# Kernel optimization log

Measured on AMD Instinct MI355X. Metric: run time of the kernel, lower is better.

## Reference

```python
import jax, jax.numpy as jnp
import numpy as np

NH, NOPE_D, ROPE_D, V_D, R = 16, 48, 16, 64, 128
EPS = 1e-6

def rms_norm(x, w):
    norm = jax.lax.rsqrt(jnp.mean(jnp.square(x), axis=-1, keepdims=True) + EPS)
    return x * norm * w

def apply_rope(x, cos, sin):
    # x: (..., rope_d); cos/sin broadcastable (..., rope_d//2)
    d = x.shape[-1]
    x1, x2 = x[..., : d // 2], x[..., d // 2 :]
    return jnp.concatenate([x1 * cos - x2 * sin, x2 * cos + x1 * sin], axis=-1)

def setup_inputs() -> dict:
    key = jax.random.key(0)
    ks = jax.random.split(key, 8)
    B, T, D = 2, 2048, 1024
    s = lambda fan_in: 1.0 / np.sqrt(fan_in)
    return {
        "x": jax.random.normal(ks[0], (B, T, D), jnp.float32),
        "cos": jax.random.uniform(ks[1], (T, ROPE_D // 2), jnp.float32),
        "sin": jax.random.uniform(ks[2], (T, ROPE_D // 2), jnp.float32),
        "Wq": jax.random.normal(ks[3], (NH * (NOPE_D + ROPE_D), D), jnp.float32) * s(D),
        "q_norm_w": jnp.ones((NOPE_D + ROPE_D,), jnp.float32),
        "Wkva": jax.random.normal(ks[4], (R + ROPE_D, D), jnp.float32) * s(D),
        "kva_norm_w": jnp.ones((R,), jnp.float32),
        "Wkvb": jax.random.normal(ks[5], (NH * (NOPE_D + V_D), R), jnp.float32) * s(R),
        "Wo": jax.random.normal(ks[6], (D, NH * V_D), jnp.float32) * s(NH * V_D),
    }

def reference(x, cos, sin, Wq, q_norm_w, Wkva, kva_norm_w, Wkvb, Wo):
    B, T, D = x.shape
    # Q path: project, per-head RMSNorm over (nope+rope) dims, split
    q = (x @ Wq.T).reshape(B, T, NH, NOPE_D + ROPE_D)
    q = rms_norm(q, q_norm_w)
    q_nope, q_rope = q[..., :NOPE_D], q[..., NOPE_D:]
    # Low-rank KV path
    kv_a = x @ Wkva.T  # (B,T,R+ROPE_D)
    kv_latent = rms_norm(kv_a[..., :R], kva_norm_w)
    k_rope_raw = kv_a[..., R:]  # (B,T,ROPE_D) shared across heads
    kv_b = (kv_latent @ Wkvb.T).reshape(B, T, NH, NOPE_D + V_D)
    k_nope, v = kv_b[..., :NOPE_D], kv_b[..., NOPE_D:]
    # Decoupled RoPE
    cos_t = cos[None, :T, None, :]  # (1,T,1,rope_d/2)
    sin_t = sin[None, :T, None, :]
    q_rope = apply_rope(q_rope, cos_t, sin_t)
    k_rope = apply_rope(k_rope_raw[:, :, None, :], cos[None, :T, None, :], sin[None, :T, None, :])
    k_rope = jnp.broadcast_to(k_rope, (B, T, NH, ROPE_D))
    q_full = jnp.concatenate([q_nope, q_rope], axis=-1)  # (B,T,NH,64)
    k_full = jnp.concatenate([k_nope, k_rope], axis=-1)
    # Causal attention, scale = 1/sqrt(nope+rope)
    scale = (NOPE_D + ROPE_D) ** -0.5
    scores = jnp.einsum("bqhd,bkhd->bhqk", q_full, k_full) * scale
    causal = jnp.tril(jnp.ones((T, T), bool))
    scores = jnp.where(causal[None, None], scores, -jnp.inf)
    attn = jax.nn.softmax(scores, axis=-1)
    out = jnp.einsum("bhqk,bkhd->bqhd", attn, v).reshape(B, T, NH * V_D)
    return out @ Wo.T
```

## Files before the change

### kernel.cpp

```cpp
#include <hip/hip_runtime.h>
#include <hip/hip_bf16.h>
#include <math.h>

#define NH 16
#define T_ 2048
#define B_ 2
#define D_ 1024
#define EPS 1e-6f

typedef __attribute__((ext_vector_type(8))) short bf16x8;
typedef __attribute__((ext_vector_type(4))) float f32x4;

__device__ __forceinline__ float wred_sum(float v){
  #pragma unroll
  for (int o = 32; o > 0; o >>= 1) v += __shfl_xor(v, o, 64);
  return v;
}

__device__ __forceinline__ unsigned pack_bf16(float a, float b){
  __hip_bfloat162 t = __float22bfloat162_rn(make_float2(a, b));
  unsigned r; __builtin_memcpy(&r, &t, 4); return r;
}

__device__ __forceinline__ void gload_lds16(const void* g, void* l){
  __builtin_amdgcn_global_load_lds((const __attribute__((address_space(1))) void*)g,
                                   (__attribute__((address_space(3))) void*)l, 16, 0, 0);
}

__global__ __launch_bounds__(256)
void cvt5(const float* __restrict__ x, const float* __restrict__ wq,
          const float* __restrict__ wkva, const float* __restrict__ wkvb,
          const float* __restrict__ wo,
          __hip_bfloat16* __restrict__ xb, __hip_bfloat16* __restrict__ wqb,
          __hip_bfloat16* __restrict__ wkvab, __hip_bfloat16* __restrict__ wkvbb,
          __hip_bfloat16* __restrict__ wob)
{
  const int i = blockIdx.x * 256 + threadIdx.x;
  const float* s; __hip_bfloat16* d; int off;
  if      (i < 1048576) { s = x;    d = xb;    off = i; }
  else if (i < 1310720) { s = wq;   d = wqb;   off = i - 1048576; }
  else if (i < 1347584) { s = wkva; d = wkvab; off = i - 1310720; }
  else if (i < 1404928) { s = wkvb; d = wkvbb; off = i - 1347584; }
  else                  { s = wo;   d = wob;   off = i - 1404928; }
  float4 v = *(const float4*)(s + (size_t)off * 4);
  *(__hip_bfloat162*)(d + (size_t)off * 4)     = __float22bfloat162_rn(make_float2(v.x, v.y));
  *(__hip_bfloat162*)(d + (size_t)off * 4 + 2) = __float22bfloat162_rn(make_float2(v.z, v.w));
}

template<typename CT>
__global__ __launch_bounds__(256, 2)
void gemm_bt64(const __hip_bfloat16* __restrict__ A, const __hip_bfloat16* __restrict__ W,
               CT* __restrict__ C, int M, int N, int K)
{
  __shared__ __hip_bfloat16 As[128 * 64];
  __shared__ __hip_bfloat16 Ws[64 * 64];
  const int tid = threadIdx.x;
  const int wv = tid >> 6, lane = tid & 63;
  const int m = lane & 15, quad = lane >> 4;
  const int bm = blockIdx.y * 128, bn = blockIdx.x * 64;

  const __hip_bfloat16* ga[4];
  const __hip_bfloat16* gw[2];
  #pragma unroll
  for (int i = 0; i < 4; i++) {
    const int slot = i*256 + tid;
    const int row = slot >> 3, cb = slot & 7;
    ga[i] = A + (size_t)(bm + row) * K + ((cb ^ (row & 7)) << 3);
  }
  #pragma unroll
  for (int i = 0; i < 2; i++) {
    const int slot = i*256 + tid;
    const int row = slot >> 3, cb = slot & 7;
    int wr = bn + row; if (wr >= N) wr = N - 1;
    gw[i] = W + (size_t)wr * K + ((cb ^ (row & 7)) << 3);
  }

  f32x4 acc[2][4];
  #pragma unroll
  for (int mi = 0; mi < 2; mi++)
    #pragma unroll
    for (int nj = 0; nj < 4; nj++) acc[mi][nj] = (f32x4){0.f,0.f,0.f,0.f};

  for (int k0 = 0; k0 < K; k0 += 64) {
    #pragma unroll
    for (int i = 0; i < 4; i++) {
      gload_lds16(ga[i], As + (i*256 + wv*64)*8);
      ga[i] += 64;
    }
    #pragma unroll
    for (int i = 0; i < 2; i++) {
      gload_lds16(gw[i], Ws + (i*256 + wv*64)*8);
      gw[i] += 64;
    }
    __syncthreads();
    #pragma unroll
    for (int ks = 0; ks < 2; ks++) {
      const int cb = ((ks*4 + quad) ^ (m & 7)) << 3;
      bf16x8 af[2], wf[4];
      #pragma unroll
      for (int mi = 0; mi < 2; mi++)
        af[mi] = *(const bf16x8*)(As + (wv*32 + mi*16 + m) * 64 + cb);
      #pragma unroll
      for (int nj = 0; nj < 4; nj++)
        wf[nj] = *(const bf16x8*)(Ws + (nj*16 + m) * 64 + cb);
      #pragma unroll
      for (int mi = 0; mi < 2; mi++)
        #pragma unroll
        for (int nj = 0; nj < 4; nj++)
          acc[mi][nj] = __builtin_amdgcn_mfma_f32_16x16x32_bf16(af[mi], wf[nj], acc[mi][nj], 0, 0, 0);
    }
    __syncthreads();
  }

  #pragma unroll
  for (int mi = 0; mi < 2; mi++)
    #pragma unroll
    for (int nj = 0; nj < 4; nj++) {
      const int col = bn + nj*16 + m;
      if (col < N) {
        #pragma unroll
        for (int r = 0; r < 4; r++) {
          const int row = bm + wv*32 + mi*16 + quad*4 + r;
          if constexpr (sizeof(CT) == 2)
            C[(size_t)row * N + col] = (CT)__float2bfloat16(acc[mi][nj][r]);
          else
            C[(size_t)row * N + col] = acc[mi][nj][r];
        }
      }
    }
}

__global__ __launch_bounds__(256, 2)
void gemm_q_fused(const __hip_bfloat16* __restrict__ A, const __hip_bfloat16* __restrict__ W,
                  const float* __restrict__ qw, const float* __restrict__ cosp,
                  const float* __restrict__ sinp, __hip_bfloat16* __restrict__ qb)
{
  __shared__ __hip_bfloat16 As[128 * 64];
  __shared__ __hip_bfloat16 Ws[64 * 64];
  const int K = 1024;
  const int tid = threadIdx.x;
  const int wv = tid >> 6, lane = tid & 63;
  const int m = lane & 15, quad = lane >> 4;
  const int bm = blockIdx.y * 128;
  const int head = blockIdx.x;
  const int bn = head * 64;

  const __hip_bfloat16* ga[4];
  const __hip_bfloat16* gw[2];
  #pragma unroll
  for (int i = 0; i < 4; i++) {
    const int slot = i*256 + tid;
    const int row = slot >> 3, cb = slot & 7;
    ga[i] = A + (size_t)(bm + row) * K + ((cb ^ (row & 7)) << 3);
  }
  #pragma unroll
  for (int i = 0; i < 2; i++) {
    const int slot = i*256 + tid;
    const int row = slot >> 3, cb = slot & 7;
    gw[i] = W + (size_t)(bn + row) * K + ((cb ^ (row & 7)) << 3);
  }

  f32x4 acc[2][4];
  #pragma unroll
  for (int mi = 0; mi < 2; mi++)
    #pragma unroll
    for (int nj = 0; nj < 4; nj++) acc[mi][nj] = (f32x4){0.f,0.f,0.f,0.f};

  for (int k0 = 0; k0 < K; k0 += 64) {
    #pragma unroll
    for (int i = 0; i < 4; i++) { gload_lds16(ga[i], As + (i*256 + wv*64)*8); ga[i] += 64; }
    #pragma unroll
    for (int i = 0; i < 2; i++) { gload_lds16(gw[i], Ws + (i*256 + wv*64)*8); gw[i] += 64; }
    __syncthreads();
    #pragma unroll
    for (int ks = 0; ks < 2; ks++) {
      const int cb = ((ks*4 + quad) ^ (m & 7)) << 3;
      bf16x8 af[2], wf[4];
      #pragma unroll
      for (int mi = 0; mi < 2; mi++)
        af[mi] = *(const bf16x8*)(As + (wv*32 + mi*16 + m) * 64 + cb);
      #pragma unroll
      for (int nj = 0; nj < 4; nj++)
        wf[nj] = *(const bf16x8*)(Ws + (nj*16 + m) * 64 + cb);
      #pragma unroll
      for (int mi = 0; mi < 2; mi++)
        #pragma unroll
        for (int nj = 0; nj < 4; nj++)
          acc[mi][nj] = __builtin_amdgcn_mfma_f32_16x16x32_bf16(af[mi], wf[nj], acc[mi][nj], 0, 0, 0);
    }
    __syncthreads();
  }

  float qwv[4];
  #pragma unroll
  for (int nj = 0; nj < 4; nj++) qwv[nj] = qw[nj*16 + m];
  const int j = m & 7;
  #pragma unroll
  for (int mi = 0; mi < 2; mi++) {
    #pragma unroll
    for (int r = 0; r < 4; r++) {
      float ss = 0.f;
      #pragma unroll
      for (int nj = 0; nj < 4; nj++) { const float t = acc[mi][nj][r]; ss = fmaf(t, t, ss); }
      ss += __shfl_xor(ss, 1, 64); ss += __shfl_xor(ss, 2, 64);
      ss += __shfl_xor(ss, 4, 64); ss += __shfl_xor(ss, 8, 64);
      const float nrm = rsqrtf(ss * (1.0f/64.0f) + EPS);
      float v[4];
      #pragma unroll
      for (int nj = 0; nj < 4; nj++) v[nj] = acc[mi][nj][r] * nrm * qwv[nj];
      const int grow = bm + wv*32 + mi*16 + quad*4 + r;
      const int t = grow & (T_ - 1);
      const int b = grow >> 11;
      const float part = __shfl_xor(v[3], 8, 64);
      const float c = cosp[t*8 + j], sn = sinp[t*8 + j];
      v[3] = (m < 8) ? (v[3]*c - part*sn) : (v[3]*c + part*sn);
      __hip_bfloat16* dst = qb + ((size_t)(b*NH + head)*T_ + t)*64 + m;
      #pragma unroll
      for (int nj = 0; nj < 4; nj++) dst[nj*16] = __float2bfloat16(v[nj] * 0.125f);
    }
  }
}

__global__ void prep_kv(const float* __restrict__ kva, const float* __restrict__ kw,
                        const float* __restrict__ cosp, const float* __restrict__ sinp,
                        __hip_bfloat16* __restrict__ kvl16, __hip_bfloat16* __restrict__ krope16)
{
  const int tid = threadIdx.x;
  const int bt = blockIdx.x;
  const int t = bt % T_;
  const float* row = kva + (size_t)bt * 144;
  const float v = row[tid];
  float s = wred_sum(v * v);
  __shared__ float red[2];
  if ((tid & 63) == 0) red[tid >> 6] = s;
  __syncthreads();
  const float total = red[0] + red[1];
  const float norm = rsqrtf(total * (1.0f/128.0f) + EPS);
  kvl16[(size_t)bt * 128 + tid] = __float2bfloat16(v * norm * kw[tid]);
  if (tid < 16) {
    const int j = tid & 7;
    const float c = cosp[t*8 + j], sn = sinp[t*8 + j];
    const float x1 = row[128 + j], x2 = row[136 + j];
    krope16[(size_t)bt * 16 + tid] = __float2bfloat16((tid < 8) ? (x1 * c - x2 * sn)
                                                               : (x2 * c + x1 * sn));
  }
}

__global__ __launch_bounds__(256)
void pack_v(const __hip_bfloat16* __restrict__ kvb16, __hip_bfloat16* __restrict__ vt)
{
  __shared__ short Vl[64][72];
  const int tid = threadIdx.x;
  const int t0 = blockIdx.x * 64;
  const int bh = blockIdx.y;
  const int b = bh >> 4, h = bh & 15;
  const int r = tid >> 2, c = tid & 3;
  {
    const short* src = (const short*)(kvb16 + ((size_t)(b*T_ + t0 + r)*1792 + h*112 + 48 + c*16));
    union { bf16x8 v; short e[8]; } u0, u1;
    u0.v = *(const bf16x8*)src;
    u1.v = *(const bf16x8*)(src + 8);
    #pragma unroll
    for (int jj = 0; jj < 8; jj++) { Vl[r][c*16+jj] = u0.e[jj]; Vl[r][c*16+8+jj] = u1.e[jj]; }
  }
  __syncthreads();
  const int d = tid >> 2, tq = tid & 3;
  union { bf16x8 v; short e[8]; } o0, o1;
  #pragma unroll
  for (int jj = 0; jj < 8; jj++) { o0.e[jj] = Vl[tq*16+jj][d]; o1.e[jj] = Vl[tq*16+8+jj][d]; }
  short* dst = (short*)(vt + ((size_t)bh*64 + d)*T_ + t0 + tq*16);
  *(bf16x8*)dst = o0.v;
  *(bf16x8*)(dst + 8) = o1.v;
}

__device__ __forceinline__ void fa_softmax(f32x4 (&s)[8], const bool diag,
    const int k0, const int qglob, const int m, const int quad,
    float& mrun, float& lrun, f32x4 (&o)[4], bf16x8 (&a)[4])
{
  if (diag) {
    #pragma unroll
    for (int sub = 0; sub < 8; sub++)
      #pragma unroll
      for (int r = 0; r < 4; r++)
        if (k0 + sub*16 + quad*4 + r > qglob) s[sub][r] = -1e30f;
  }
  float tm = -3.0e38f;
  #pragma unroll
  for (int sub = 0; sub < 8; sub++)
    #pragma unroll
    for (int r = 0; r < 4; r++) tm = fmaxf(tm, s[sub][r]);
  tm = fmaxf(tm, __shfl_xor(tm, 16, 64));
  tm = fmaxf(tm, __shfl_xor(tm, 32, 64));
  const float mn = fmaxf(mrun, tm);
  const float alpha = __expf(mrun - mn);
  float rs = 0.f;
  float p[8][4];
  #pragma unroll
  for (int sub = 0; sub < 8; sub++)
    #pragma unroll
    for (int r = 0; r < 4; r++) {
      const float e = __expf(s[sub][r] - mn);
      p[sub][r] = e; rs += e;
    }
  rs += __shfl_xor(rs, 16, 64);
  rs += __shfl_xor(rs, 32, 64);
  lrun = lrun * alpha + rs;
  mrun = mn;

  unsigned u[8][2];
  #pragma unroll
  for (int sub = 0; sub < 8; sub++) {
    u[sub][0] = pack_bf16(p[sub][0], p[sub][1]);
    u[sub][1] = pack_bf16(p[sub][2], p[sub][3]);
  }
  #pragma unroll
  for (int c = 0; c < 4; c++) {
    union { int i[4]; bf16x8 v; } au;
    #pragma unroll
    for (int w4 = 0; w4 < 4; w4++) {
      const int src = (((2*quad + (w4 >> 1)) & 3) << 4) | m;
      const int lo = __shfl((int)u[c*2][w4 & 1], src, 64);
      const int hi = __shfl((int)u[c*2+1][w4 & 1], src, 64);
      au.i[w4] = (quad & 2) ? hi : lo;
    }
    a[c] = au.v;
  }

  float al[4];
  #pragma unroll
  for (int r = 0; r < 4; r++) al[r] = __shfl(alpha, (quad << 2) | r, 64);
  #pragma unroll
  for (int vs = 0; vs < 4; vs++)
    #pragma unroll
    for (int r = 0; r < 4; r++) o[vs][r] *= al[r];
}

__device__ __forceinline__ void fa_store(float lrun, f32x4 (&oacc)[4],
    const int b, const int qrow0, const int h, const int m, const int quad,
    __hip_bfloat16* __restrict__ aout)
{
  float lr[4];
  #pragma unroll
  for (int r = 0; r < 4; r++) lr[r] = __shfl(lrun, (quad << 2) | r, 64);
  #pragma unroll
  for (int vs = 0; vs < 4; vs++)
    #pragma unroll
    for (int r = 0; r < 4; r++)
      aout[(size_t)(b*T_ + qrow0 + quad*4 + r) * 1024 + h*64 + vs*16 + m]
          = __float2bfloat16(oacc[vs][r] / lr[r]);
}

__global__ __launch_bounds__(256, 2)
void attn_pair2(const __hip_bfloat16* __restrict__ qb,
                const __hip_bfloat16* __restrict__ kvb16,
                const __hip_bfloat16* __restrict__ krope16,
                const __hip_bfloat16* __restrict__ vt16,
                __hip_bfloat16* __restrict__ aout)
{
  __shared__ __hip_bfloat16 SL[32768];
  const int tid = threadIdx.x;
  const int wv = tid >> 6, lane = tid & 63;
  const int m = lane & 15, quad = lane >> 4;
  const int ta = blockIdx.x;
  const int tb = 31 - ta;
  const int bh = blockIdx.y;
  const int b = bh >> 4, h = bh & 15;
  const int qbaseA = ta*64 + wv*16;
  const int qbaseB = tb*64 + wv*16;
  const int ntA = (ta + 2) >> 1;
  const int ntB = (tb + 2) >> 1;

  const __hip_bfloat16* qra = qb + ((size_t)bh*T_ + qbaseA + m)*64 + quad*8;
  const bf16x8 qA0 = *(const bf16x8*)qra, qA1 = *(const bf16x8*)(qra + 32);
  const __hip_bfloat16* qrb = qb + ((size_t)bh*T_ + qbaseB + m)*64 + quad*8;
  const bf16x8 qB0 = *(const bf16x8*)qrb, qB1 = *(const bf16x8*)(qrb + 32);

  const __hip_bfloat16* pK[4]; size_t iK[4];
  const __hip_bfloat16* pV[4];
  #pragma unroll
  for (int i = 0; i < 4; i++) {
    const int slot = i*256 + tid;
    const int krow = slot >> 3;
    const int kde = (slot & 7) ^ (krow & 7);
    if (kde < 6) { pK[i] = kvb16 + (size_t)(b*T_ + krow)*1792 + h*112 + kde*8; iK[i] = (size_t)128*1792; }
    else         { pK[i] = krope16 + (size_t)(b*T_ + krow)*16 + (kde-6)*8;     iK[i] = (size_t)128*16; }
    const int vd = slot >> 4;
    const int vde = (slot & 15) ^ (vd & 7);
    pV[i] = vt16 + ((size_t)bh*64 + vd)*T_ + vde*8;
  }

  auto stage = [&](int buf){
    #pragma unroll
    for (int i = 0; i < 4; i++) {
      gload_lds16(pK[i], SL + buf*8192 + (i*256 + wv*64)*8);
      gload_lds16(pV[i], SL + 16384 + buf*8192 + (i*256 + wv*64)*8);
      pK[i] += iK[i]; pV[i] += 128;
    }
  };

  f32x4 oA[4], oB[4];
  #pragma unroll
  for (int vs = 0; vs < 4; vs++) { oA[vs] = (f32x4){0.f,0.f,0.f,0.f}; oB[vs] = (f32x4){0.f,0.f,0.f,0.f}; }
  float mA = -3.0e38f, lA = 0.f, mB = -3.0e38f, lB = 0.f;

  const int sw0 = quad ^ (m & 7);
  stage(0);

  for (int kt = 0; kt < ntB; kt++) {
    const int cur = kt & 1;
    __syncthreads();
    const __hip_bfloat16* Kc = SL + cur*8192;
    const __hip_bfloat16* Vc = SL + 16384 + cur*8192;
    const bool doA = (kt < ntA);

    f32x4 sA[8], sB[8];
    #pragma unroll
    for (int sub = 0; sub < 8; sub++) {
      const bf16x8 kf0 = *(const bf16x8*)(Kc + (sub*16 + m)*64 + sw0*8);
      const bf16x8 kf1 = *(const bf16x8*)(Kc + (sub*16 + m)*64 + (sw0^4)*8);
      f32x4 z = (f32x4){0.f,0.f,0.f,0.f};
      z = __builtin_amdgcn_mfma_f32_16x16x32_bf16(kf0, qB0, z, 0, 0, 0);
      z = __builtin_amdgcn_mfma_f32_16x16x32_bf16(kf1, qB1, z, 0, 0, 0);
      sB[sub] = z;
      if (doA) {
        f32x4 y = (f32x4){0.f,0.f,0.f,0.f};
        y = __builtin_amdgcn_mfma_f32_16x16x32_bf16(kf0, qA0, y, 0, 0, 0);
        y = __builtin_amdgcn_mfma_f32_16x16x32_bf16(kf1, qA1, y, 0, 0, 0);
        sA[sub] = y;
      }
    }

    if (kt + 1 < ntB) stage(cur ^ 1);

    bf16x8 aA[4], aB[4];
    fa_softmax(sB, kt == ntB-1, kt*128, qbaseB + m, m, quad, mB, lB, oB, aB);
    if (doA) fa_softmax(sA, kt == ntA-1, kt*128, qbaseA + m, m, quad, mA, lA, oA, aA);

    #pragma unroll
    for (int vs = 0; vs < 4; vs++) {
      #pragma unroll
      for (int c = 0; c < 4; c++) {
        const bf16x8 vf = *(const bf16x8*)(Vc + (vs*16 + m)*128 + (((c*4 + quad) ^ (m & 7)) << 3));
        oB[vs] = __builtin_amdgcn_mfma_f32_16x16x32_bf16(aB[c], vf, oB[vs], 0, 0, 0);
        if (doA) oA[vs] = __builtin_amdgcn_mfma_f32_16x16x32_bf16(aA[c], vf, oA[vs], 0, 0, 0);
      }
    }
  }

  fa_store(lA, oA, b, qbaseA, h, m, quad, aout);
  fa_store(lB, oB, b, qbaseB, h, m, quad, aout);
}

extern "C" void kernel_launch(void* const* d_in, const int* in_sizes, int n_in,
                              void* d_out, int out_size, void* d_ws, size_t ws_size,
                              hipStream_t stream)
{
  const float* x    = (const float*)d_in[0];
  const float* cosp = (const float*)d_in[1];
  const float* sinp = (const float*)d_in[2];
  const float* Wq   = (const float*)d_in[3];
  const float* qw   = (const float*)d_in[4];
  const float* Wkva = (const float*)d_in[5];
  const float* kw   = (const float*)d_in[6];
  const float* Wkvb = (const float*)d_in[7];
  const float* Wo   = (const float*)d_in[8];
  float* out = (float*)d_out;

  float* kva = (float*)d_ws;
  __hip_bfloat16* kvb16   = (__hip_bfloat16*)(kva + 589824);
  __hip_bfloat16* kvl16   = kvb16 + 7340032;
  __hip_bfloat16* qb16    = kvl16 + 524288;
  __hip_bfloat16* vt16    = qb16 + 4194304;
  __hip_bfloat16* krope16 = vt16 + 4194304;
  __hip_bfloat16* Wqb     = krope16 + 65536;
  __hip_bfloat16* Wkvab   = Wqb + 1048576;
  __hip_bfloat16* Wkvbb   = Wkvab + 147456;
  __hip_bfloat16* Wob     = Wkvbb + 229376;
  __hip_bfloat16* ab16    = Wob + 1048576;
  __hip_bfloat16* xb16    = kvb16;

  const int M = B_ * T_;

  cvt5<<<6512, 256, 0, stream>>>(x, Wq, Wkva, Wkvb, Wo, xb16, Wqb, Wkvab, Wkvbb, Wob);
  gemm_q_fused<<<dim3(16, 32), 256, 0, stream>>>(xb16, Wqb, qw, cosp, sinp, qb16);
  gemm_bt64<float><<<dim3(3, 32), 256, 0, stream>>>(xb16, Wkvab, kva, M, 144, 1024);
  prep_kv<<<M, 128, 0, stream>>>(kva, kw, cosp, sinp, kvl16, krope16);
  gemm_bt64<__hip_bfloat16><<<dim3(28, 32), 256, 0, stream>>>(kvl16, Wkvbb, kvb16, M, 1792, 128);
  pack_v<<<dim3(T_/64, B_ * NH), 256, 0, stream>>>(kvb16, vt16);
  attn_pair2<<<dim3(16, B_ * NH), 256, 0, stream>>>(qb16, kvb16, krope16, vt16, ab16);
  gemm_bt64<float><<<dim3(16, 32), 256, 0, stream>>>(ab16, Wob, out, M, 1024, 1024);
}
```

Baseline: 209.7 us.

## Fuse Q and KV-A GEMMs, double-buffer GEMMs, fuse V transpose into KV-B GEMM

Merges the Q projection and the KV-A projection into one launch that picks its weight matrix by block index. All GEMMs now double-buffer their LDS tiles, so the next K slice loads while the current one computes, and one barrier per iteration is removed. Wkvb rows are permuted during the bf16 conversion so the KV-B GEMM writes k_nope as a compact array and writes V already transposed through LDS. This removes the separate pack_v kernel and the large kvb intermediate. The cost is twice the LDS per block, which may lower occupancy, plus a more involved epilogue.

```diff
diff --git a/kernel.cpp b/kernel.cpp
--- a/kernel.cpp
+++ b/kernel.cpp
@@ -36,15 +36,21 @@
           __hip_bfloat16* __restrict__ wob)
 {
   const int i = blockIdx.x * 256 + threadIdx.x;
-  const float* s; __hip_bfloat16* d; int off;
-  if      (i < 1048576) { s = x;    d = xb;    off = i; }
-  else if (i < 1310720) { s = wq;   d = wqb;   off = i - 1048576; }
-  else if (i < 1347584) { s = wkva; d = wkvab; off = i - 1310720; }
-  else if (i < 1404928) { s = wkvb; d = wkvbb; off = i - 1347584; }
-  else                  { s = wo;   d = wob;   off = i - 1404928; }
-  float4 v = *(const float4*)(s + (size_t)off * 4);
-  *(__hip_bfloat162*)(d + (size_t)off * 4)     = __float22bfloat162_rn(make_float2(v.x, v.y));
-  *(__hip_bfloat162*)(d + (size_t)off * 4 + 2) = __float22bfloat162_rn(make_float2(v.z, v.w));
+  const float* s; __hip_bfloat16* d; size_t soff, doff;
+  if      (i < 1048576) { s = x;    d = xb;    soff = doff = i; }
+  else if (i < 1310720) { s = wq;   d = wqb;   soff = doff = i - 1048576; }
+  else if (i < 1347584) { s = wkva; d = wkvab; soff = doff = i - 1310720; }
+  else if (i < 1404928) {
+    const int off = i - 1347584;
+    const int srow = off >> 5, c4 = off & 31;
+    const int h = srow / 112, dd = srow % 112;
+    const int drow = (dd < 48) ? (h*48 + dd) : (768 + h*64 + (dd - 48));
+    s = wkvb; d = wkvbb; soff = off; doff = (size_t)drow*32 + c4;
+  }
+  else                  { s = wo;   d = wob;   soff = doff = i - 1404928; }
+  float4 v = *(const float4*)(s + soff * 4);
+  *(__hip_bfloat162*)(d + doff * 4)     = __float22bfloat162_rn(make_float2(v.x, v.y));
+  *(__hip_bfloat162*)(d + doff * 4 + 2) = __float22bfloat162_rn(make_float2(v.z, v.w));
 }
 
 template<typename CT>
@@ -52,8 +58,8 @@
 void gemm_bt64(const __hip_bfloat16* __restrict__ A, const __hip_bfloat16* __restrict__ W,
                CT* __restrict__ C, int M, int N, int K)
 {
-  __shared__ __hip_bfloat16 As[128 * 64];
-  __shared__ __hip_bfloat16 Ws[64 * 64];
+  __shared__ __hip_bfloat16 As[2][128 * 64];
+  __shared__ __hip_bfloat16 Ws[2][64 * 64];
   const int tid = threadIdx.x;
   const int wv = tid >> 6, lane = tid & 63;
   const int m = lane & 15, quad = lane >> 4;
@@ -74,6 +80,12 @@
     int wr = bn + row; if (wr >= N) wr = N - 1;
     gw[i] = W + (size_t)wr * K + ((cb ^ (row & 7)) << 3);
   }
+  auto stage = [&](int buf){
+    #pragma unroll
+    for (int i = 0; i < 4; i++) { gload_lds16(ga[i], &As[buf][(i*256 + wv*64)*8]); ga[i] += 64; }
+    #pragma unroll
+    for (int i = 0; i < 2; i++) { gload_lds16(gw[i], &Ws[buf][(i*256 + wv*64)*8]); gw[i] += 64; }
+  };
 
   f32x4 acc[2][4];
   #pragma unroll
@@ -81,35 +93,28 @@
     #pragma unroll
     for (int nj = 0; nj < 4; nj++) acc[mi][nj] = (f32x4){0.f,0.f,0.f,0.f};
 
-  for (int k0 = 0; k0 < K; k0 += 64) {
-    #pragma unroll
-    for (int i = 0; i < 4; i++) {
-      gload_lds16(ga[i], As + (i*256 + wv*64)*8);
-      ga[i] += 64;
-    }
-    #pragma unroll
-    for (int i = 0; i < 2; i++) {
-      gload_lds16(gw[i], Ws + (i*256 + wv*64)*8);
-      gw[i] += 64;
-    }
+  stage(0);
+  const int iters = K >> 6;
+  for (int it = 0; it < iters; it++) {
+    const int cur = it & 1;
     __syncthreads();
+    if (it + 1 < iters) stage(cur ^ 1);
     #pragma unroll
     for (int ks = 0; ks < 2; ks++) {
       const int cb = ((ks*4 + quad) ^ (m & 7)) << 3;
       bf16x8 af[2], wf[4];
       #pragma unroll
       for (int mi = 0; mi < 2; mi++)
-        af[mi] = *(const bf16x8*)(As + (wv*32 + mi*16 + m) * 64 + cb);
+        af[mi] = *(const bf16x8*)(&As[cur][(wv*32 + mi*16 + m) * 64 + cb]);
       #pragma unroll
       for (int nj = 0; nj < 4; nj++)
-        wf[nj] = *(const bf16x8*)(Ws + (nj*16 + m) * 64 + cb);
+        wf[nj] = *(const bf16x8*)(&Ws[cur][(nj*16 + m) * 64 + cb]);
       #pragma unroll
       for (int mi = 0; mi < 2; mi++)
         #pragma unroll
         for (int nj = 0; nj < 4; nj++)
           acc[mi][nj] = __builtin_amdgcn_mfma_f32_16x16x32_bf16(af[mi], wf[nj], acc[mi][nj], 0, 0, 0);
     }
-    __syncthreads();
   }
 
   #pragma unroll
@@ -131,19 +136,23 @@
 }
 
 __global__ __launch_bounds__(256, 2)
-void gemm_q_fused(const __hip_bfloat16* __restrict__ A, const __hip_bfloat16* __restrict__ W,
-                  const float* __restrict__ qw, const float* __restrict__ cosp,
-                  const float* __restrict__ sinp, __hip_bfloat16* __restrict__ qb)
-{
-  __shared__ __hip_bfloat16 As[128 * 64];
-  __shared__ __hip_bfloat16 Ws[64 * 64];
+void gemm_qkva(const __hip_bfloat16* __restrict__ A, const __hip_bfloat16* __restrict__ Wqb,
+               const __hip_bfloat16* __restrict__ Wkvab,
+               const float* __restrict__ qw, const float* __restrict__ cosp,
+               const float* __restrict__ sinp,
+               __hip_bfloat16* __restrict__ qb, float* __restrict__ kva)
+{
+  __shared__ __hip_bfloat16 As[2][128 * 64];
+  __shared__ __hip_bfloat16 Ws[2][64 * 64];
   const int K = 1024;
   const int tid = threadIdx.x;
   const int wv = tid >> 6, lane = tid & 63;
   const int m = lane & 15, quad = lane >> 4;
   const int bm = blockIdx.y * 128;
-  const int head = blockIdx.x;
-  const int bn = head * 64;
+  const bool isq = blockIdx.x < 16;
+  const __hip_bfloat16* W = isq ? Wqb : Wkvab;
+  const int bn = isq ? blockIdx.x*64 : (blockIdx.x - 16)*64;
+  const int Nw = isq ? 1024 : 144;
 
   const __hip_bfloat16* ga[4];
   const __hip_bfloat16* gw[2];
@@ -157,8 +166,15 @@
   for (int i = 0; i < 2; i++) {
     const int slot = i*256 + tid;
     const int row = slot >> 3, cb = slot & 7;
-    gw[i] = W + (size_t)(bn + row) * K + ((cb ^ (row & 7)) << 3);
-  }
+    int wr = bn + row; if (wr >= Nw) wr = Nw - 1;
+    gw[i] = W + (size_t)wr * K + ((cb ^ (row & 7)) << 3);
+  }
+  auto stage = [&](int buf){
+    #pragma unroll
+    for (int i = 0; i < 4; i++) { gload_lds16(ga[i], &As[buf][(i*256 + wv*64)*8]); ga[i] += 64; }
+    #pragma unroll
+    for (int i = 0; i < 2; i++) { gload_lds16(gw[i], &Ws[buf][(i*256 + wv*64)*8]); gw[i] += 64; }
+  };
 
   f32x4 acc[2][4];
   #pragma unroll
@@ -166,58 +182,73 @@
     #pragma unroll
     for (int nj = 0; nj < 4; nj++) acc[mi][nj] = (f32x4){0.f,0.f,0.f,0.f};
 
-  for (int k0 = 0; k0 < K; k0 += 64) {
-    #pragma unroll
-    for (int i = 0; i < 4; i++) { gload_lds16(ga[i], As + (i*256 + wv*64)*8); ga[i] += 64; }
-    #pragma unroll
-    for (int i = 0; i < 2; i++) { gload_lds16(gw[i], Ws + (i*256 + wv*64)*8); gw[i] += 64; }
+  stage(0);
+  for (int it = 0; it < 16; it++) {
+    const int cur = it & 1;
     __syncthreads();
+    if (it < 15) stage(cur ^ 1);
     #pragma unroll
     for (int ks = 0; ks < 2; ks++) {
       const int cb = ((ks*4 + quad) ^ (m & 7)) << 3;
       bf16x8 af[2], wf[4];
       #pragma unroll
       for (int mi = 0; mi < 2; mi++)
-        af[mi] = *(const bf16x8*)(As + (wv*32 + mi*16 + m) * 64 + cb);
+        af[mi] = *(const bf16x8*)(&As[cur][(wv*32 + mi*16 + m) * 64 + cb]);
       #pragma unroll
       for (int nj = 0; nj < 4; nj++)
-        wf[nj] = *(const bf16x8*)(Ws + (nj*16 + m) * 64 + cb);
+        wf[nj] = *(const bf16x8*)(&Ws[cur][(nj*16 + m) * 64 + cb]);
       #pragma unroll
       for (int mi = 0; mi < 2; mi++)
         #pragma unroll
         for (int nj = 0; nj < 4; nj++)
           acc[mi][nj] = __builtin_amdgcn_mfma_f32_16x16x32_bf16(af[mi], wf[nj], acc[mi][nj], 0, 0, 0);
     }
-    __syncthreads();
-  }
-
-  float qwv[4];
-  #pragma unroll
-  for (int nj = 0; nj < 4; nj++) qwv[nj] = qw[nj*16 + m];
-  const int j = m & 7;
-  #pragma unroll
-  for (int mi = 0; mi < 2; mi++) {
-    #pragma unroll
-    for (int r = 0; r < 4; r++) {
-      float ss = 0.f;
-      #pragma unroll
-      for (int nj = 0; nj < 4; nj++) { const float t = acc[mi][nj][r]; ss = fmaf(t, t, ss); }
-      ss += __shfl_xor(ss, 1, 64); ss += __shfl_xor(ss, 2, 64);
-      ss += __shfl_xor(ss, 4, 64); ss += __shfl_xor(ss, 8, 64);
-      const float nrm = rsqrtf(ss * (1.0f/64.0f) + EPS);
-      float v[4];
-      #pragma unroll
-      for (int nj = 0; nj < 4; nj++) v[nj] = acc[mi][nj][r] * nrm * qwv[nj];
-      const int grow = bm + wv*32 + mi*16 + quad*4 + r;
-      const int t = grow & (T_ - 1);
-      const int b = grow >> 11;
-      const float part = __shfl_xor(v[3], 8, 64);
-      const float c = cosp[t*8 + j], sn = sinp[t*8 + j];
-      v[3] = (m < 8) ? (v[3]*c - part*sn) : (v[3]*c + part*sn);
-      __hip_bfloat16* dst = qb + ((size_t)(b*NH + head)*T_ + t)*64 + m;
-      #pragma unroll
-      for (int nj = 0; nj < 4; nj++) dst[nj*16] = __float2bfloat16(v[nj] * 0.125f);
-    }
+  }
+
+  if (isq) {
+    const int head = blockIdx.x;
+    float qwv[4];
+    #pragma unroll
+    for (int nj = 0; nj < 4; nj++) qwv[nj] = qw[nj*16 + m];
+    const int j = m & 7;
+    #pragma unroll
+    for (int mi = 0; mi < 2; mi++) {
+      #pragma unroll
+      for (int r = 0; r < 4; r++) {
+        float ss = 0.f;
+        #pragma unroll
+        for (int nj = 0; nj < 4; nj++) { const float t = acc[mi][nj][r]; ss = fmaf(t, t, ss); }
+        ss += __shfl_xor(ss, 1, 64); ss += __shfl_xor(ss, 2, 64);
+        ss += __shfl_xor(ss, 4, 64); ss += __shfl_xor(ss, 8, 64);
+        const float nrm = rsqrtf(ss * (1.0f/64.0f) + EPS);
+        float v[4];
+        #pragma unroll
+        for (int nj = 0; nj < 4; nj++) v[nj] = acc[mi][nj][r] * nrm * qwv[nj];
+        const int grow = bm + wv*32 + mi*16 + quad*4 + r;
+        const int t = grow & (T_ - 1);
+        const int b = grow >> 11;
+        const float part = __shfl_xor(v[3], 8, 64);
+        const float c = cosp[t*8 + j], sn = sinp[t*8 + j];
+        v[3] = (m < 8) ? (v[3]*c - part*sn) : (v[3]*c + part*sn);
+        __hip_bfloat16* dst = qb + ((size_t)(b*NH + head)*T_ + t)*64 + m;
+        #pragma unroll
+        for (int nj = 0; nj < 4; nj++) dst[nj*16] = __float2bfloat16(v[nj] * 0.125f);
+      }
+    }
+  } else {
+    #pragma unroll
+    for (int mi = 0; mi < 2; mi++)
+      #pragma unroll
+      for (int nj = 0; nj < 4; nj++) {
+        const int col = bn + nj*16 + m;
+        if (col < 144) {
+          #pragma unroll
+          for (int r = 0; r < 4; r++) {
+            const int row = bm + wv*32 + mi*16 + quad*4 + r;
+            kva[(size_t)row * 144 + col] = acc[mi][nj][r];
+          }
+        }
+      }
   }
 }
 
@@ -246,31 +277,108 @@
   }
 }
 
-__global__ __launch_bounds__(256)
-void pack_v(const __hip_bfloat16* __restrict__ kvb16, __hip_bfloat16* __restrict__ vt)
-{
-  __shared__ short Vl[64][72];
+__global__ __launch_bounds__(256, 2)
+void gemm_kvb(const __hip_bfloat16* __restrict__ A, const __hip_bfloat16* __restrict__ W,
+              __hip_bfloat16* __restrict__ knope, __hip_bfloat16* __restrict__ vt)
+{
+  __shared__ __hip_bfloat16 As[2][128 * 64];
+  __shared__ __hip_bfloat16 Ws[2][64 * 64];
+  const int K = 128;
   const int tid = threadIdx.x;
-  const int t0 = blockIdx.x * 64;
-  const int bh = blockIdx.y;
-  const int b = bh >> 4, h = bh & 15;
-  const int r = tid >> 2, c = tid & 3;
-  {
-    const short* src = (const short*)(kvb16 + ((size_t)(b*T_ + t0 + r)*1792 + h*112 + 48 + c*16));
-    union { bf16x8 v; short e[8]; } u0, u1;
-    u0.v = *(const bf16x8*)src;
-    u1.v = *(const bf16x8*)(src + 8);
-    #pragma unroll
-    for (int jj = 0; jj < 8; jj++) { Vl[r][c*16+jj] = u0.e[jj]; Vl[r][c*16+8+jj] = u1.e[jj]; }
-  }
-  __syncthreads();
-  const int d = tid >> 2, tq = tid & 3;
-  union { bf16x8 v; short e[8]; } o0, o1;
-  #pragma unroll
-  for (int jj = 0; jj < 8; jj++) { o0.e[jj] = Vl[tq*16+jj][d]; o1.e[jj] = Vl[tq*16+8+jj][d]; }
-  short* dst = (short*)(vt + ((size_t)bh*64 + d)*T_ + t0 + tq*16);
-  *(bf16x8*)dst = o0.v;
-  *(bf16x8*)(dst + 8) = o1.v;
+  const int wv = tid >> 6, lane = tid & 63;
+  const int m = lane & 15, quad = lane >> 4;
+  const int bm = blockIdx.y * 128, bn = blockIdx.x * 64;
+
+  const __hip_bfloat16* ga[4];
+  const __hip_bfloat16* gw[2];
+  #pragma unroll
+  for (int i = 0; i < 4; i++) {
+    const int slot = i*256 + tid;
+    const int row = slot >> 3, cb = slot & 7;
+    ga[i] = A + (size_t)(bm + row) * K + ((cb ^ (row & 7)) << 3);
+  }
+  #pragma unroll
+  for (int i = 0; i < 2; i++) {
+    const int slot = i*256 + tid;
+    const int row = slot >> 3, cb = slot & 7;
+    gw[i] = W + (size_t)(bn + row) * K + ((cb ^ (row & 7)) << 3);
+  }
+  auto stage = [&](int buf){
+    #pragma unroll
+    for (int i = 0; i < 4; i++) { gload_lds16(ga[i], &As[buf][(i*256 + wv*64)*8]); ga[i] += 64; }
+    #pragma unroll
+    for (int i = 0; i < 2; i++) { gload_lds16(gw[i], &Ws[buf][(i*256 + wv*64)*8]); gw[i] += 64; }
+  };
+
+  f32x4 acc[2][4];
+  #pragma unroll
+  for (int mi = 0; mi < 2; mi++)
+    #pragma unroll
+    for (int nj = 0; nj < 4; nj++) acc[mi][nj] = (f32x4){0.f,0.f,0.f,0.f};
+
+  stage(0);
+  for (int it = 0; it < 2; it++) {
+    const int cur = it & 1;
+    __syncthreads();
+    if (it == 0) stage(1);
+    #pragma unroll
+    for (int ks = 0; ks < 2; ks++) {
+      const int cb = ((ks*4 + quad) ^ (m & 7)) << 3;
+      bf16x8 af[2], wf[4];
+      #pragma unroll
+      for (int mi = 0; mi < 2; mi++)
+        af[mi] = *(const bf16x8*)(&As[cur][(wv*32 + mi*16 + m) * 64 + cb]);
+      #pragma unroll
+      for (int nj = 0; nj < 4; nj++)
+        wf[nj] = *(const bf16x8*)(&Ws[cur][(nj*16 + m) * 64 + cb]);
+      #pragma unroll
+      for (int mi = 0; mi < 2; mi++)
+        #pragma unroll
+        for (int nj = 0; nj < 4; nj++)
+          acc[mi][nj] = __builtin_amdgcn_mfma_f32_16x16x32_bf16(af[mi], wf[nj], acc[mi][nj], 0, 0, 0);
+    }
+  }
+
+  if (bn < 768) {
+    #pragma unroll
+    for (int mi = 0; mi < 2; mi++)
+      #pragma unroll
+      for (int nj = 0; nj < 4; nj++) {
+        const int col = bn + nj*16 + m;
+        #pragma unroll
+        for (int r = 0; r < 4; r++) {
+          const int row = bm + wv*32 + mi*16 + quad*4 + r;
+          knope[(size_t)row * 768 + col] = __float2bfloat16(acc[mi][nj][r]);
+        }
+      }
+  } else {
+    __syncthreads();
+    short* TL = (short*)&As[0][0];
+    #pragma unroll
+    for (int mi = 0; mi < 2; mi++)
+      #pragma unroll
+      for (int nj = 0; nj < 4; nj++) {
+        const int d = nj*16 + m;
+        #pragma unroll
+        for (int r = 0; r < 4; r++) {
+          const int tl = wv*32 + mi*16 + quad*4 + r;
+          __hip_bfloat16 hv = __float2bfloat16(acc[mi][nj][r]);
+          short sv; __builtin_memcpy(&sv, &hv, 2);
+          TL[d*136 + tl] = sv;
+        }
+      }
+    __syncthreads();
+    const int h = (bn - 768) >> 6;
+    const int b = bm >> 11;
+    const int t0 = bm & (T_ - 1);
+    #pragma unroll
+    for (int i = 0; i < 4; i++) {
+      const int unit = i*256 + tid;
+      const int d = unit >> 4, tu = unit & 15;
+      *(bf16x8*)(vt + ((size_t)(b*NH + h)*64 + d)*T_ + t0 + tu*8)
+          = *(const bf16x8*)(TL + d*136 + tu*8);
+    }
+  }
 }
 
 __device__ __forceinline__ void fa_softmax(f32x4 (&s)[8], const bool diag,
@@ -352,7 +460,7 @@
 
 __global__ __launch_bounds__(256, 2)
 void attn_pair2(const __hip_bfloat16* __restrict__ qb,
-                const __hip_bfloat16* __restrict__ kvb16,
+                const __hip_bfloat16* __restrict__ knope,
                 const __hip_bfloat16* __restrict__ krope16,
                 const __hip_bfloat16* __restrict__ vt16,
                 __hip_bfloat16* __restrict__ aout)
@@ -382,8 +490,8 @@
     const int slot = i*256 + tid;
     const int krow = slot >> 3;
     const int kde = (slot & 7) ^ (krow & 7);
-    if (kde < 6) { pK[i] = kvb16 + (size_t)(b*T_ + krow)*1792 + h*112 + kde*8; iK[i] = (size_t)128*1792; }
-    else         { pK[i] = krope16 + (size_t)(b*T_ + krow)*16 + (kde-6)*8;     iK[i] = (size_t)128*16; }
+    if (kde < 6) { pK[i] = knope + (size_t)(b*T_ + krow)*768 + h*48 + kde*8; iK[i] = (size_t)128*768; }
+    else         { pK[i] = krope16 + (size_t)(b*T_ + krow)*16 + (kde-6)*8;   iK[i] = (size_t)128*16; }
     const int vd = slot >> 4;
     const int vde = (slot & 15) ^ (vd & 7);
     pV[i] = vt16 + ((size_t)bh*64 + vd)*T_ + vde*8;
@@ -467,8 +575,9 @@
   float* out = (float*)d_out;
 
   float* kva = (float*)d_ws;
-  __hip_bfloat16* kvb16   = (__hip_bfloat16*)(kva + 589824);
-  __hip_bfloat16* kvl16   = kvb16 + 7340032;
+  __hip_bfloat16* xb16    = (__hip_bfloat16*)(kva + 589824);
+  __hip_bfloat16* knope16 = xb16 + 4194304;
+  __hip_bfloat16* kvl16   = knope16 + 3145728;
   __hip_bfloat16* qb16    = kvl16 + 524288;
   __hip_bfloat16* vt16    = qb16 + 4194304;
   __hip_bfloat16* krope16 = vt16 + 4194304;
@@ -477,16 +586,13 @@
   __hip_bfloat16* Wkvbb   = Wkvab + 147456;
   __hip_bfloat16* Wob     = Wkvbb + 229376;
   __hip_bfloat16* ab16    = Wob + 1048576;
-  __hip_bfloat16* xb16    = kvb16;
 
   const int M = B_ * T_;
 
   cvt5<<<6512, 256, 0, stream>>>(x, Wq, Wkva, Wkvb, Wo, xb16, Wqb, Wkvab, Wkvbb, Wob);
-  gemm_q_fused<<<dim3(16, 32), 256, 0, stream>>>(xb16, Wqb, qw, cosp, sinp, qb16);
-  gemm_bt64<float><<<dim3(3, 32), 256, 0, stream>>>(xb16, Wkvab, kva, M, 144, 1024);
+  gemm_qkva<<<dim3(19, 32), 256, 0, stream>>>(xb16, Wqb, Wkvab, qw, cosp, sinp, qb16, kva);
   prep_kv<<<M, 128, 0, stream>>>(kva, kw, cosp, sinp, kvl16, krope16);
-  gemm_bt64<__hip_bfloat16><<<dim3(28, 32), 256, 0, stream>>>(kvl16, Wkvbb, kvb16, M, 1792, 128);
-  pack_v<<<dim3(T_/64, B_ * NH), 256, 0, stream>>>(kvb16, vt16);
-  attn_pair2<<<dim3(16, B_ * NH), 256, 0, stream>>>(qb16, kvb16, krope16, vt16, ab16);
+  gemm_kvb<<<dim3(28, 32), 256, 0, stream>>>(kvl16, Wkvbb, knope16, vt16);
+  attn_pair2<<<dim3(16, B_ * NH), 256, 0, stream>>>(qb16, knope16, krope16, vt16, ab16);
   gemm_bt64<float><<<dim3(16, 32), 256, 0, stream>>>(ab16, Wob, out, M, 1024, 1024);
 }
```

Measured after the change: 190.8 us. 9.0% less time.
